# Kernel tuning notes

Hardware: AMD Instinct MI355X
Metric: run time of the kernel (lower is better)

The kernel has to match this reference:

```python
import jax, jax.numpy as jnp
import numpy as np

N, E, D = 10000, 160000, 512
H, C = 4, 128          # hidden layers: 4 heads x 128 = 512 (residual-compatible)
HF, CF = 2, 512        # final layer: 2 heads, concat=False (mean)
NEG_SLOPE = 0.2


def _gat(x, src, dst, W, a_src, a_dst, b, heads, out_c, concat):
    """PyG-style GATConv (v1 attention), no dropout (eval mode)."""
    n = x.shape[0]
    h = (x @ W).reshape(n, heads, out_c)                  # [N,H,C]
    es = (h * a_src).sum(-1)                              # [N,H]
    ed = (h * a_dst).sum(-1)                              # [N,H]
    e = jax.nn.leaky_relu(es[src] + ed[dst], NEG_SLOPE)   # [E,H]
    m = jax.ops.segment_max(e, dst, num_segments=n)       # softmax over in-edges of dst
    m = jnp.where(jnp.isfinite(m), m, 0.0)                # guard isolated nodes
    ex = jnp.exp(e - m[dst])
    den = jax.ops.segment_sum(ex, dst, num_segments=n)
    alpha = ex / (den[dst] + 1e-16)                       # [E,H]
    msg = h[src] * alpha[..., None]                       # [E,H,C]
    out = jax.ops.segment_sum(msg, dst, num_segments=n)   # [N,H,C]
    out = out.reshape(n, heads * out_c) if concat else out.mean(axis=1)
    return out + b


def setup_inputs() -> dict:
    key = jax.random.key(0)
    ks = jax.random.split(key, 16)
    s = 0.05
    return {
        "graph": jax.random.normal(ks[0], (N, D), jnp.float32),
        "edge_index": jax.random.randint(ks[1], (2, E), 0, N, dtype=jnp.int32),
        "W1": jax.random.normal(ks[2], (D, H * C), jnp.float32) * s,
        "as1": jax.random.normal(ks[3], (H, C), jnp.float32) * s,
        "ad1": jax.random.normal(ks[4], (H, C), jnp.float32) * s,
        "b1": jnp.zeros((H * C,), jnp.float32),
        "W2": jax.random.normal(ks[5], (H * C, H * C), jnp.float32) * s,
        "as2": jax.random.normal(ks[6], (H, C), jnp.float32) * s,
        "ad2": jax.random.normal(ks[7], (H, C), jnp.float32) * s,
        "b2": jnp.zeros((H * C,), jnp.float32),
        "W3": jax.random.normal(ks[8], (H * C, HF * CF), jnp.float32) * s,
        "as3": jax.random.normal(ks[9], (HF, CF), jnp.float32) * s,
        "ad3": jax.random.normal(ks[10], (HF, CF), jnp.float32) * s,
        "b3": jnp.zeros((CF,), jnp.float32),
    }


def reference(graph, edge_index, W1, as1, ad1, b1, W2, as2, ad2, b2, W3, as3, ad3, b3):
    src, dst = edge_index[0], edge_index[1]
    # layer_size=2: conv1 + convs[0] with ELU+residual, convs[1] (concat=False) residual only
    x = jax.nn.elu(_gat(graph, src, dst, W1, as1, ad1, b1, H, C, True) + graph)
    x = jax.nn.elu(_gat(x, src, dst, W2, as2, ad2, b2, H, C, True) + x)
    x = _gat(x, src, dst, W3, as3, ad3, b3, HF, CF, False) + x
    return x
```

## Files before the change

kernel.cpp:

```cpp
#include <hip/hip_runtime.h>
#include <hip/hip_bf16.h>
#include <hip/hip_fp16.h>
#include <cstddef>
#include <cstdint>


typedef _Float16 half8 __attribute__((ext_vector_type(8)));
typedef _Float16 half4v __attribute__((ext_vector_type(4)));
typedef _Float16 half2v __attribute__((ext_vector_type(2)));
typedef float floatx4 __attribute__((ext_vector_type(4)));

#define AS1(p) ((const __attribute__((address_space(1))) void*)(p))
#define AS3(p) ((__attribute__((address_space(3))) void*)(p))


__global__ void count_deg(const int* __restrict__ dst, int* __restrict__ deg, int E) {
    int e = blockIdx.x * blockDim.x + threadIdx.x;
    if (e < E) atomicAdd(&deg[dst[e]], 1);
}

__global__ void scan_kernel(const int* __restrict__ deg, int* __restrict__ row_start,
                            int* __restrict__ cursor, int n) {
    __shared__ int wsum[16];
    __shared__ int carry_s;
    int tid = threadIdx.x;
    int wave = tid >> 6, lane = tid & 63;
    if (tid == 0) { carry_s = 0; row_start[0] = 0; }
    __syncthreads();
    for (int base = 0; base < n; base += 1024) {
        int i = base + tid;
        int v = (i < n) ? deg[i] : 0;
        int x = v;
#pragma unroll
        for (int off = 1; off < 64; off <<= 1) {
            int t = __shfl_up(x, off);
            if (lane >= off) x += t;
        }
        if (lane == 63) wsum[wave] = x;
        __syncthreads();
        if (wave == 0 && lane < 16) {
            int w = wsum[lane];
#pragma unroll
            for (int off = 1; off < 16; off <<= 1) {
                int t = __shfl_up(w, off);
                if (lane >= off) w += t;
            }
            wsum[lane] = w;
        }
        __syncthreads();
        int carry = carry_s;
        int incl = x + (wave ? wsum[wave - 1] : 0) + carry;
        if (i < n) { row_start[i + 1] = incl; cursor[i] = incl - v; }
        __syncthreads();
        if (tid == 1023) carry_s = incl;
        __syncthreads();
    }
}

__global__ void scatter_edges(const int* __restrict__ src, const int* __restrict__ dst,
                              int* __restrict__ cursor, int* __restrict__ srcs, int E) {
    int e = blockIdx.x * blockDim.x + threadIdx.x;
    if (e < E) {
        int p = atomicAdd(&cursor[dst[e]], 1);
        srcs[p] = src[e];
    }
}


__global__ void cast_f16(const float* __restrict__ in, _Float16* __restrict__ out, int n4) {
    int i = blockIdx.x * blockDim.x + threadIdx.x;
    if (i < n4) {
        float4 v = ((const float4*)in)[i];
        half4v o = {(_Float16)v.x, (_Float16)v.y, (_Float16)v.z, (_Float16)v.w};
        ((half4v*)out)[i] = o;
    }
}

__global__ void transpose_cast_g(const float* __restrict__ in, _Float16* __restrict__ out,
                                 int R, int Cc, int in_ld, int out_ld) {
    __shared__ float t[32][33];
    int r0 = blockIdx.y * 32, c0 = blockIdx.x * 32;
    int tx = threadIdx.x, ty = threadIdx.y;
    for (int i = ty; i < 32; i += 8)
        t[i][tx] = in[(size_t)(r0 + i) * in_ld + c0 + tx];
    __syncthreads();
    for (int i = ty; i < 32; i += 8)
        out[(size_t)(c0 + i) * out_ld + r0 + tx] = (_Float16)t[tx][i];
}


#define BK 64

__global__ __launch_bounds__(256) void gemm_f16(const _Float16* __restrict__ A,
                                                const _Float16* __restrict__ Bt,
                                                _Float16* __restrict__ C,
                                                int M, int Nn, int K) {
    __shared__ _Float16 As[64 * BK];
    __shared__ _Float16 Bs[64 * BK];
    int tid = threadIdx.x;
    int lane = tid & 63, wave = tid >> 6;
    int wm = (wave & 1) * 32, wn = (wave >> 1) * 32;
    int m0 = blockIdx.y * 64, n0 = blockIdx.x * 64;
    int l15 = lane & 15, quad = lane >> 4;
    int trow = tid >> 3, tcol = tid & 7;

    floatx4 acc[2][2];
#pragma unroll
    for (int i = 0; i < 2; ++i)
#pragma unroll
        for (int j = 0; j < 2; ++j) acc[i][j] = (floatx4){0.f, 0.f, 0.f, 0.f};

    for (int k0 = 0; k0 < K; k0 += BK) {
        __syncthreads();
#pragma unroll
        for (int i = 0; i < 2; ++i) {
            int gr = m0 + i * 32 + trow; if (gr >= M) gr = M - 1;
            __builtin_amdgcn_global_load_lds(AS1(A + (size_t)gr * K + k0 + tcol * 8),
                                             AS3(As + (size_t)(i * 256 + tid) * 8), 16, 0, 0);
        }
#pragma unroll
        for (int i = 0; i < 2; ++i) {
            int gr = n0 + i * 32 + trow;
            __builtin_amdgcn_global_load_lds(AS1(Bt + (size_t)gr * K + k0 + tcol * 8),
                                             AS3(Bs + (size_t)(i * 256 + tid) * 8), 16, 0, 0);
        }
        __syncthreads();
#pragma unroll
        for (int ks = 0; ks < BK; ks += 32) {
            half8 af[2], bfr[2];
#pragma unroll
            for (int i = 0; i < 2; ++i)
                af[i] = *(const half8*)&As[(wm + i * 16 + l15) * BK + ks + quad * 8];
#pragma unroll
            for (int j = 0; j < 2; ++j)
                bfr[j] = *(const half8*)&Bs[(wn + j * 16 + l15) * BK + ks + quad * 8];
#pragma unroll
            for (int i = 0; i < 2; ++i)
#pragma unroll
                for (int j = 0; j < 2; ++j)
                    acc[i][j] = __builtin_amdgcn_mfma_f32_16x16x32_f16(af[i], bfr[j], acc[i][j], 0, 0, 0);
        }
    }
#pragma unroll
    for (int i = 0; i < 2; ++i)
#pragma unroll
        for (int j = 0; j < 2; ++j) {
            int col = n0 + wn + j * 16 + l15;
#pragma unroll
            for (int r = 0; r < 4; ++r) {
                int row = m0 + wm + i * 16 + quad * 4 + r;
                if (row < M) C[(size_t)row * Nn + col] = (_Float16)acc[i][j][r];
            }
        }
}

__global__ __launch_bounds__(256) void gemm_f16_ep(const _Float16* __restrict__ A,
                                                   const _Float16* __restrict__ Bt,
                                                   float* __restrict__ out,
                                                   const float* __restrict__ bias,
                                                   const float* __restrict__ xres,
                                                   int M, int Nn, int K) {
    __shared__ _Float16 As[64 * BK];
    __shared__ _Float16 Bs[64 * BK];
    int tid = threadIdx.x;
    int lane = tid & 63, wave = tid >> 6;
    int wm = (wave & 1) * 32, wn = (wave >> 1) * 32;
    int m0 = blockIdx.y * 64, n0 = blockIdx.x * 64;
    int l15 = lane & 15, quad = lane >> 4;
    int trow = tid >> 3, tcol = tid & 7;

    floatx4 acc[2][2];
#pragma unroll
    for (int i = 0; i < 2; ++i)
#pragma unroll
        for (int j = 0; j < 2; ++j) acc[i][j] = (floatx4){0.f, 0.f, 0.f, 0.f};

    for (int k0 = 0; k0 < K; k0 += BK) {
        __syncthreads();
#pragma unroll
        for (int i = 0; i < 2; ++i) {
            int gr = m0 + i * 32 + trow; if (gr >= M) gr = M - 1;
            __builtin_amdgcn_global_load_lds(AS1(A + (size_t)gr * K + k0 + tcol * 8),
                                             AS3(As + (size_t)(i * 256 + tid) * 8), 16, 0, 0);
        }
#pragma unroll
        for (int i = 0; i < 2; ++i) {
            int gr = n0 + i * 32 + trow;
            __builtin_amdgcn_global_load_lds(AS1(Bt + (size_t)gr * K + k0 + tcol * 8),
                                             AS3(Bs + (size_t)(i * 256 + tid) * 8), 16, 0, 0);
        }
        __syncthreads();
#pragma unroll
        for (int ks = 0; ks < BK; ks += 32) {
            half8 af[2], bfr[2];
#pragma unroll
            for (int i = 0; i < 2; ++i)
                af[i] = *(const half8*)&As[(wm + i * 16 + l15) * BK + ks + quad * 8];
#pragma unroll
            for (int j = 0; j < 2; ++j)
                bfr[j] = *(const half8*)&Bs[(wn + j * 16 + l15) * BK + ks + quad * 8];
#pragma unroll
            for (int i = 0; i < 2; ++i)
#pragma unroll
                for (int j = 0; j < 2; ++j)
                    acc[i][j] = __builtin_amdgcn_mfma_f32_16x16x32_f16(af[i], bfr[j], acc[i][j], 0, 0, 0);
        }
    }
#pragma unroll
    for (int i = 0; i < 2; ++i)
#pragma unroll
        for (int j = 0; j < 2; ++j) {
            int col = n0 + wn + j * 16 + l15;
#pragma unroll
            for (int r = 0; r < 4; ++r) {
                int row = m0 + wm + i * 16 + quad * 4 + r;
                if (row < M)
                    out[(size_t)row * Nn + col] =
                        0.5f * acc[i][j][r] + bias[col] + xres[(size_t)row * Nn + col];
            }
        }
}


__global__ void attn_coef(const _Float16* __restrict__ h, const float* __restrict__ a_src,
                          const float* __restrict__ a_dst, float* __restrict__ es,
                          float* __restrict__ ed, int NH, int Hh, int C) {
    int gw = (blockIdx.x * blockDim.x + threadIdx.x) >> 6;
    int lane = threadIdx.x & 63;
    if (gw >= NH) return;
    int hd = gw % Hh;
    const _Float16* hp = h + (size_t)gw * C;
    const float* ap = a_src + hd * C;
    const float* dp = a_dst + hd * C;
    float ss = 0.f, sd = 0.f;
    for (int c = lane; c < C; c += 64) {
        float hv = (float)hp[c];
        ss += hv * ap[c];
        sd += hv * dp[c];
    }
#pragma unroll
    for (int off = 32; off; off >>= 1) {
        ss += __shfl_down(ss, off);
        sd += __shfl_down(sd, off);
    }
    if (lane == 0) { es[gw] = ss; ed[gw] = sd; }
}

__global__ void attn_coef_shared(const _Float16* __restrict__ x, const float* __restrict__ a_src,
                                 const float* __restrict__ a_dst, float* __restrict__ es,
                                 float* __restrict__ ed, int NH, int Hh, int C) {
    int gw = (blockIdx.x * blockDim.x + threadIdx.x) >> 6;
    int lane = threadIdx.x & 63;
    if (gw >= NH) return;
    int n = gw / Hh, hd = gw - n * Hh;
    const _Float16* hp = x + (size_t)n * C;
    const float* ap = a_src + hd * C;
    const float* dp = a_dst + hd * C;
    float ss = 0.f, sd = 0.f;
    for (int c = lane; c < C; c += 64) {
        float hv = (float)hp[c];
        ss += hv * ap[c];
        sd += hv * dp[c];
    }
#pragma unroll
    for (int off = 32; off; off >>= 1) {
        ss += __shfl_down(ss, off);
        sd += __shfl_down(sd, off);
    }
    if (lane == 0) { es[gw] = ss; ed[gw] = sd; }
}

__global__ void proj_a3(const float* __restrict__ W3, const float* __restrict__ as3,
                        const float* __restrict__ ad3, float* __restrict__ wes,
                        float* __restrict__ wed) {
    int gw = (blockIdx.x * blockDim.x + threadIdx.x) >> 6;
    int lane = threadIdx.x & 63;
    int k = gw & 511, h = (gw >> 9) & 1, sel = gw >> 10;
    const float* a = (sel ? ad3 : as3) + h * 512;
    const float* row = W3 + (size_t)k * 1024 + h * 512;
    float s = 0.f;
    for (int c = lane; c < 512; c += 64) s += row[c] * a[c];
#pragma unroll
    for (int off = 32; off; off >>= 1) s += __shfl_down(s, off);
    if (lane == 0) (sel ? wed : wes)[h * 512 + k] = s;
}


template <int H>
__global__ __launch_bounds__(256) void attn_alpha_packed(
    const float* __restrict__ es, const float* __restrict__ ed,
    const int* __restrict__ row_start, const int* __restrict__ srcs,
    float* __restrict__ alpha, int Nn, int E) {
    const int EP = 64 / H;
    int wave = threadIdx.x >> 6, lane = threadIdx.x & 63;
    int n = blockIdx.x * 4 + wave;
    if (n >= Nn) return;
    int h = lane & (H - 1);
    int eslot = lane / H;
    float edn = ed[n * H + h];
    int beg = row_start[n], end = row_start[n + 1];
    float m = -INFINITY;
    for (int j0 = beg; j0 < end; j0 += EP) {
        int j = j0 + eslot;
        float e = -INFINITY;
        if (j < end) {
            e = es[srcs[j] * H + h] + edn;
            e = (e > 0.f) ? e : 0.2f * e;
            alpha[(size_t)h * E + j] = e;
        }
        m = fmaxf(m, e);
    }
#pragma unroll
    for (int off = H; off < 64; off <<= 1) m = fmaxf(m, __shfl_xor(m, off));
    float den = 0.f;
    for (int j0 = beg; j0 < end; j0 += EP) {
        int j = j0 + eslot;
        if (j < end) {
            float w = __expf(alpha[(size_t)h * E + j] - m);
            alpha[(size_t)h * E + j] = w;
            den += w;
        }
    }
#pragma unroll
    for (int off = H; off < 64; off <<= 1) den += __shfl_xor(den, off);
    float inv = 1.f / (den + 1e-16f);
    for (int j0 = beg; j0 < end; j0 += EP) {
        int j = j0 + eslot;
        if (j < end) alpha[(size_t)h * E + j] *= inv;
    }
}


__global__ __launch_bounds__(512) void aggregate3_concat(
    const _Float16* __restrict__ h, const float* __restrict__ alpha,
    const int* __restrict__ row_start, const int* __restrict__ srcs,
    const float* __restrict__ bias, const float* __restrict__ x_res,
    float* __restrict__ x_out, _Float16* __restrict__ x_out_h, int E) {
    __shared__ float red[8][512];
    int n = blockIdx.x;
    int tid = threadIdx.x;
    int slot = tid >> 6, lane = tid & 63;
    int head = lane >> 4;
    int c0 = lane * 8;
    const float* al = alpha + (size_t)head * E;
    int beg = row_start[n], end = row_start[n + 1];
    float acc[8] = {};
    int j = beg + slot;
    for (; j + 8 < end; j += 16) {
        int s0 = srcs[j], s1 = srcs[j + 8];
        float w0 = al[j], w1 = al[j + 8];
        half8 h0 = *(const half8*)&h[(size_t)s0 * 512 + c0];
        half8 h1 = *(const half8*)&h[(size_t)s1 * 512 + c0];
#pragma unroll
        for (int k = 0; k < 8; ++k) acc[k] += w0 * (float)h0[k];
#pragma unroll
        for (int k = 0; k < 8; ++k) acc[k] += w1 * (float)h1[k];
    }
    if (j < end) {
        int s = srcs[j];
        float w = al[j];
        half8 hv = *(const half8*)&h[(size_t)s * 512 + c0];
#pragma unroll
        for (int k = 0; k < 8; ++k) acc[k] += w * (float)hv[k];
    }
#pragma unroll
    for (int k = 0; k < 8; ++k) red[slot][c0 + k] = acc[k];
    __syncthreads();
    int c = tid;
    size_t base = (size_t)n * 512 + c;
    float v = red[0][c] + red[1][c] + red[2][c] + red[3][c] +
              red[4][c] + red[5][c] + red[6][c] + red[7][c] + bias[c] + x_res[base];
    v = (v > 0.f) ? v : expm1f(v);
    x_out[base] = v;
    x_out_h[base] = (_Float16)v;
}


__global__ __launch_bounds__(512) void aggregate_x_dual(
    const _Float16* __restrict__ x, const float* __restrict__ alpha,
    const int* __restrict__ row_start, const int* __restrict__ srcs,
    _Float16* __restrict__ y, int E) {
    __shared__ float red[8][1024];
    int n = blockIdx.x;
    int tid = threadIdx.x;
    int slot = tid >> 6, lane = tid & 63;
    int c0 = lane * 8;
    const float* al0 = alpha;
    const float* al1 = alpha + E;
    int beg = row_start[n], end = row_start[n + 1];
    float a0[8] = {}, a1[8] = {};
    int j = beg + slot;
    for (; j + 8 < end; j += 16) {
        int s0 = srcs[j], s1 = srcs[j + 8];
        float u0 = al0[j], v0 = al1[j];
        float u1 = al0[j + 8], v1 = al1[j + 8];
        half8 h0 = *(const half8*)&x[(size_t)s0 * 512 + c0];
        half8 h1 = *(const half8*)&x[(size_t)s1 * 512 + c0];
#pragma unroll
        for (int k = 0; k < 8; ++k) {
            float f = (float)h0[k];
            a0[k] += u0 * f;
            a1[k] += v0 * f;
        }
#pragma unroll
        for (int k = 0; k < 8; ++k) {
            float f = (float)h1[k];
            a0[k] += u1 * f;
            a1[k] += v1 * f;
        }
    }
    if (j < end) {
        int s = srcs[j];
        float u = al0[j], v = al1[j];
        half8 hv = *(const half8*)&x[(size_t)s * 512 + c0];
#pragma unroll
        for (int k = 0; k < 8; ++k) {
            float f = (float)hv[k];
            a0[k] += u * f;
            a1[k] += v * f;
        }
    }
#pragma unroll
    for (int k = 0; k < 8; ++k) {
        red[slot][c0 + k] = a0[k];
        red[slot][512 + c0 + k] = a1[k];
    }
    __syncthreads();
    int c = tid * 2;
    half2v o;
#pragma unroll
    for (int k = 0; k < 2; ++k) {
        float s = red[0][c + k] + red[1][c + k] + red[2][c + k] + red[3][c + k] +
                  red[4][c + k] + red[5][c + k] + red[6][c + k] + red[7][c + k];
        o[k] = (_Float16)s;
    }
    *(half2v*)&y[(size_t)n * 1024 + c] = o;
}


extern "C" void kernel_launch(void* const* d_in, const int* in_sizes, int n_in,
                              void* d_out, int out_size, void* d_ws, size_t ws_size,
                              hipStream_t stream) {
    const float* graph = (const float*)d_in[0];
    const int* edge_index = (const int*)d_in[1];
    const float* W1 = (const float*)d_in[2];
    const float* as1 = (const float*)d_in[3];
    const float* ad1 = (const float*)d_in[4];
    const float* b1 = (const float*)d_in[5];
    const float* W2 = (const float*)d_in[6];
    const float* as2 = (const float*)d_in[7];
    const float* ad2 = (const float*)d_in[8];
    const float* b2 = (const float*)d_in[9];
    const float* W3 = (const float*)d_in[10];
    const float* as3 = (const float*)d_in[11];
    const float* ad3 = (const float*)d_in[12];
    const float* b3 = (const float*)d_in[13];

    const int D = 512;
    int N = in_sizes[0] / D;
    int E = in_sizes[1] / 2;
    const int* src = edge_index;
    const int* dst = edge_index + E;

    char* p = (char*)d_ws;
    auto carve = [&](size_t bytes) {
        void* r = (void*)p;
        p += (bytes + 255) & ~(size_t)255;
        return r;
    };
    _Float16* Ah  = (_Float16*)carve((size_t)N * 512 * 2);
    _Float16* Wt  = (_Float16*)carve((size_t)512 * 512 * 2);
    _Float16* Bt3 = (_Float16*)carve((size_t)512 * 1024 * 2);
    _Float16* h_h = (_Float16*)carve((size_t)N * 1024 * 2);
    float* x1     = (float*)carve((size_t)N * 512 * 4);
    float* x2     = (float*)carve((size_t)N * 512 * 4);
    float* es     = (float*)carve((size_t)N * 4 * 4);
    float* ed     = (float*)carve((size_t)N * 4 * 4);
    float* alpha  = (float*)carve((size_t)4 * E * 4);
    float* wes3   = (float*)carve((size_t)2 * 512 * 4);
    float* wed3   = (float*)carve((size_t)2 * 512 * 4);
    int* deg      = (int*)carve((size_t)N * 4);
    int* cur      = (int*)carve((size_t)N * 4);
    int* row_st   = (int*)carve((size_t)(N + 1) * 4);
    int* srcs     = (int*)carve((size_t)E * 4);

    hipMemsetAsync(deg, 0, (size_t)N * 4, stream);
    count_deg<<<(E + 255) / 256, 256, 0, stream>>>(dst, deg, E);
    scan_kernel<<<1, 1024, 0, stream>>>(deg, row_st, cur, N);
    scatter_edges<<<(E + 255) / 256, 256, 0, stream>>>(src, dst, cur, srcs, E);

    cast_f16<<<(N * 512 / 4 + 255) / 256, 256, 0, stream>>>(graph, Ah, N * 512 / 4);

    dim3 tblk(32, 8);
    int nblk4 = (N + 3) / 4;
    int mblk = (N + 63) / 64;
    transpose_cast_g<<<dim3(16, 16), tblk, 0, stream>>>(W1, Wt, 512, 512, 512, 512);
    gemm_f16<<<dim3(512 / 64, mblk), 256, 0, stream>>>(Ah, Wt, h_h, N, 512, 512);
    attn_coef<<<(N * 4 + 3) / 4, 256, 0, stream>>>(h_h, as1, ad1, es, ed, N * 4, 4, 128);
    attn_alpha_packed<4><<<nblk4, 256, 0, stream>>>(es, ed, row_st, srcs, alpha, N, E);
    aggregate3_concat<<<N, 512, 0, stream>>>(h_h, alpha, row_st, srcs, b1, graph, x1, Ah, E);

    transpose_cast_g<<<dim3(16, 16), tblk, 0, stream>>>(W2, Wt, 512, 512, 512, 512);
    gemm_f16<<<dim3(512 / 64, mblk), 256, 0, stream>>>(Ah, Wt, h_h, N, 512, 512);
    attn_coef<<<(N * 4 + 3) / 4, 256, 0, stream>>>(h_h, as2, ad2, es, ed, N * 4, 4, 128);
    attn_alpha_packed<4><<<nblk4, 256, 0, stream>>>(es, ed, row_st, srcs, alpha, N, E);
    aggregate3_concat<<<N, 512, 0, stream>>>(h_h, alpha, row_st, srcs, b2, x1, x2, Ah, E);

    transpose_cast_g<<<dim3(16, 16), tblk, 0, stream>>>(W3, Bt3, 512, 512, 1024, 1024);
    transpose_cast_g<<<dim3(16, 16), tblk, 0, stream>>>(W3 + 512, Bt3 + 512, 512, 512, 1024, 1024);
    proj_a3<<<512, 256, 0, stream>>>(W3, as3, ad3, wes3, wed3);
    attn_coef_shared<<<(N * 2 + 3) / 4, 256, 0, stream>>>(Ah, wes3, wed3, es, ed, N * 2, 2, 512);
    attn_alpha_packed<2><<<nblk4, 256, 0, stream>>>(es, ed, row_st, srcs, alpha, N, E);
    aggregate_x_dual<<<N, 512, 0, stream>>>(Ah, alpha, row_st, srcs, h_h, E);
    gemm_f16_ep<<<dim3(512 / 64, mblk), 256, 0, stream>>>(
        h_h, Bt3, (float*)d_out, b3, x2, N, 512, 1024);
}
```

Measured before the change: 347.5 us.

## Fold attention projections into GEMM columns and defer softmax normalization to aggregation

Precomputes W·a_src and W·a_dst as extra rows of the transposed weight, so the hidden-layer GEMM emits es/ed directly and the separate attention-coefficient kernels go away. The softmax kernel now writes the per-node denominator instead of renormalizing every alpha, and the aggregation kernels divide by it. Layer-3 coefficients are computed inside the layer-2 aggregation epilogue. The fp32 intermediate activations are dropped in favor of fp16 residuals, which saves bandwidth at some cost in precision. All weight preprocessing is grouped up front into a single projection kernel.

```diff
diff --git a/kernel.cpp b/kernel.cpp
--- a/kernel.cpp
+++ b/kernel.cpp
@@ -77,7 +77,7 @@
 }
 
 __global__ void transpose_cast_g(const float* __restrict__ in, _Float16* __restrict__ out,
-                                 int R, int Cc, int in_ld, int out_ld) {
+                                 int in_ld, int out_ld) {
     __shared__ float t[32][33];
     int r0 = blockIdx.y * 32, c0 = blockIdx.x * 32;
     int tx = threadIdx.x, ty = threadIdx.y;
@@ -88,13 +88,61 @@
         out[(size_t)(c0 + i) * out_ld + r0 + tx] = (_Float16)t[tx][i];
 }
 
+__global__ void proj_all(const float* __restrict__ W1, const float* __restrict__ as1,
+                         const float* __restrict__ ad1,
+                         const float* __restrict__ W2, const float* __restrict__ as2,
+                         const float* __restrict__ ad2,
+                         const float* __restrict__ W3, const float* __restrict__ as3,
+                         const float* __restrict__ ad3,
+                         _Float16* __restrict__ Wt1, _Float16* __restrict__ Wt2,
+                         float* __restrict__ wes3, float* __restrict__ wed3) {
+    int w = (blockIdx.x * blockDim.x + threadIdx.x) >> 6;
+    int lane = threadIdx.x & 63;
+    if (w < 8192) {
+        int layer = w >> 12;
+        int idx = w & 4095;
+        int d = idx & 511, hh = (idx >> 9) & 3, sel = idx >> 11;
+        const float* W = layer ? W2 : W1;
+        const float* a = layer ? (sel ? ad2 : as2) : (sel ? ad1 : as1);
+        const float* row = W + (size_t)d * 512 + hh * 128;
+        const float* av = a + hh * 128;
+        float s = 0.f;
+        s += row[lane] * av[lane];
+        s += row[lane + 64] * av[lane + 64];
+#pragma unroll
+        for (int off = 32; off; off >>= 1) s += __shfl_down(s, off);
+        if (lane == 0) {
+            _Float16* Wt = layer ? Wt2 : Wt1;
+            Wt[(size_t)(512 + sel * 4 + hh) * 512 + d] = (_Float16)s;
+        }
+    } else if (w < 10240) {
+        int idx = w - 8192;
+        int k = idx & 511, hh = (idx >> 9) & 1, sel = idx >> 10;
+        const float* a = (sel ? ad3 : as3) + hh * 512;
+        const float* row = W3 + (size_t)k * 1024 + hh * 512;
+        float s = 0.f;
+        for (int c = lane; c < 512; c += 64) s += row[c] * a[c];
+#pragma unroll
+        for (int off = 32; off; off >>= 1) s += __shfl_down(s, off);
+        if (lane == 0) (sel ? wed3 : wes3)[hh * 512 + k] = s;
+    } else if (w < 11136) {
+        int z = (w - 10240) * 64 + lane;
+        int layer = z / 28672;
+        int rem = z - layer * 28672;
+        int row = 520 + rem / 512, col = rem & 511;
+        (layer ? Wt2 : Wt1)[(size_t)row * 512 + col] = (_Float16)0.f;
+    }
+}
+
 
 #define BK 64
 
-__global__ __launch_bounds__(256) void gemm_f16(const _Float16* __restrict__ A,
-                                                const _Float16* __restrict__ Bt,
-                                                _Float16* __restrict__ C,
-                                                int M, int Nn, int K) {
+__global__ __launch_bounds__(256) void gemm_f16_att(const _Float16* __restrict__ A,
+                                                    const _Float16* __restrict__ Bt,
+                                                    _Float16* __restrict__ Hout,
+                                                    float* __restrict__ es,
+                                                    float* __restrict__ ed,
+                                                    int M, int K) {
     __shared__ _Float16 As[64 * BK];
     __shared__ _Float16 Bs[64 * BK];
     int tid = threadIdx.x;
@@ -149,7 +197,12 @@
 #pragma unroll
             for (int r = 0; r < 4; ++r) {
                 int row = m0 + wm + i * 16 + quad * 4 + r;
-                if (row < M) C[(size_t)row * Nn + col] = (_Float16)acc[i][j][r];
+                if (row < M) {
+                    float v = acc[i][j][r];
+                    if (col < 512) Hout[(size_t)row * 512 + col] = (_Float16)v;
+                    else if (col < 516) es[row * 4 + col - 512] = v;
+                    else if (col < 520) ed[row * 4 + col - 516] = v;
+                }
             }
         }
 }
@@ -158,7 +211,7 @@
                                                    const _Float16* __restrict__ Bt,
                                                    float* __restrict__ out,
                                                    const float* __restrict__ bias,
-                                                   const float* __restrict__ xres,
+                                                   const _Float16* __restrict__ xres,
                                                    int M, int Nn, int K) {
     __shared__ _Float16 As[64 * BK];
     __shared__ _Float16 Bs[64 * BK];
@@ -216,81 +269,17 @@
                 int row = m0 + wm + i * 16 + quad * 4 + r;
                 if (row < M)
                     out[(size_t)row * Nn + col] =
-                        0.5f * acc[i][j][r] + bias[col] + xres[(size_t)row * Nn + col];
+                        0.5f * acc[i][j][r] + bias[col] + (float)xres[(size_t)row * Nn + col];
             }
         }
 }
 
 
-__global__ void attn_coef(const _Float16* __restrict__ h, const float* __restrict__ a_src,
-                          const float* __restrict__ a_dst, float* __restrict__ es,
-                          float* __restrict__ ed, int NH, int Hh, int C) {
-    int gw = (blockIdx.x * blockDim.x + threadIdx.x) >> 6;
-    int lane = threadIdx.x & 63;
-    if (gw >= NH) return;
-    int hd = gw % Hh;
-    const _Float16* hp = h + (size_t)gw * C;
-    const float* ap = a_src + hd * C;
-    const float* dp = a_dst + hd * C;
-    float ss = 0.f, sd = 0.f;
-    for (int c = lane; c < C; c += 64) {
-        float hv = (float)hp[c];
-        ss += hv * ap[c];
-        sd += hv * dp[c];
-    }
-#pragma unroll
-    for (int off = 32; off; off >>= 1) {
-        ss += __shfl_down(ss, off);
-        sd += __shfl_down(sd, off);
-    }
-    if (lane == 0) { es[gw] = ss; ed[gw] = sd; }
-}
-
-__global__ void attn_coef_shared(const _Float16* __restrict__ x, const float* __restrict__ a_src,
-                                 const float* __restrict__ a_dst, float* __restrict__ es,
-                                 float* __restrict__ ed, int NH, int Hh, int C) {
-    int gw = (blockIdx.x * blockDim.x + threadIdx.x) >> 6;
-    int lane = threadIdx.x & 63;
-    if (gw >= NH) return;
-    int n = gw / Hh, hd = gw - n * Hh;
-    const _Float16* hp = x + (size_t)n * C;
-    const float* ap = a_src + hd * C;
-    const float* dp = a_dst + hd * C;
-    float ss = 0.f, sd = 0.f;
-    for (int c = lane; c < C; c += 64) {
-        float hv = (float)hp[c];
-        ss += hv * ap[c];
-        sd += hv * dp[c];
-    }
-#pragma unroll
-    for (int off = 32; off; off >>= 1) {
-        ss += __shfl_down(ss, off);
-        sd += __shfl_down(sd, off);
-    }
-    if (lane == 0) { es[gw] = ss; ed[gw] = sd; }
-}
-
-__global__ void proj_a3(const float* __restrict__ W3, const float* __restrict__ as3,
-                        const float* __restrict__ ad3, float* __restrict__ wes,
-                        float* __restrict__ wed) {
-    int gw = (blockIdx.x * blockDim.x + threadIdx.x) >> 6;
-    int lane = threadIdx.x & 63;
-    int k = gw & 511, h = (gw >> 9) & 1, sel = gw >> 10;
-    const float* a = (sel ? ad3 : as3) + h * 512;
-    const float* row = W3 + (size_t)k * 1024 + h * 512;
-    float s = 0.f;
-    for (int c = lane; c < 512; c += 64) s += row[c] * a[c];
-#pragma unroll
-    for (int off = 32; off; off >>= 1) s += __shfl_down(s, off);
-    if (lane == 0) (sel ? wed : wes)[h * 512 + k] = s;
-}
-
-
 template <int H>
-__global__ __launch_bounds__(256) void attn_alpha_packed(
+__global__ __launch_bounds__(256) void attn_alpha2(
     const float* __restrict__ es, const float* __restrict__ ed,
     const int* __restrict__ row_start, const int* __restrict__ srcs,
-    float* __restrict__ alpha, int Nn, int E) {
+    float* __restrict__ alpha, float* __restrict__ den, int Nn, int E) {
     const int EP = 64 / H;
     int wave = threadIdx.x >> 6, lane = threadIdx.x & 63;
     int n = blockIdx.x * 4 + wave;
@@ -312,31 +301,32 @@
     }
 #pragma unroll
     for (int off = H; off < 64; off <<= 1) m = fmaxf(m, __shfl_xor(m, off));
-    float den = 0.f;
+    float dsum = 0.f;
     for (int j0 = beg; j0 < end; j0 += EP) {
         int j = j0 + eslot;
         if (j < end) {
             float w = __expf(alpha[(size_t)h * E + j] - m);
             alpha[(size_t)h * E + j] = w;
-            den += w;
-        }
-    }
-#pragma unroll
-    for (int off = H; off < 64; off <<= 1) den += __shfl_xor(den, off);
-    float inv = 1.f / (den + 1e-16f);
-    for (int j0 = beg; j0 < end; j0 += EP) {
-        int j = j0 + eslot;
-        if (j < end) alpha[(size_t)h * E + j] *= inv;
-    }
-}
-
-
-__global__ __launch_bounds__(512) void aggregate3_concat(
+            dsum += w;
+        }
+    }
+#pragma unroll
+    for (int off = H; off < 64; off <<= 1) dsum += __shfl_xor(dsum, off);
+    if (lane < H) den[n * H + lane] = dsum;
+}
+
+
+template <bool RES32, bool COEF3>
+__global__ __launch_bounds__(512) void aggregate4_concat(
     const _Float16* __restrict__ h, const float* __restrict__ alpha,
+    const float* __restrict__ den,
     const int* __restrict__ row_start, const int* __restrict__ srcs,
-    const float* __restrict__ bias, const float* __restrict__ x_res,
-    float* __restrict__ x_out, _Float16* __restrict__ x_out_h, int E) {
+    const float* __restrict__ bias, const float* __restrict__ xres32,
+    const _Float16* __restrict__ xres16, _Float16* __restrict__ x_out_h,
+    const float* __restrict__ wes3, const float* __restrict__ wed3,
+    float* __restrict__ es3, float* __restrict__ ed3, int E) {
     __shared__ float red[8][512];
+    __shared__ float csum[8][4];
     int n = blockIdx.x;
     int tid = threadIdx.x;
     int slot = tid >> 6, lane = tid & 63;
@@ -367,17 +357,46 @@
     for (int k = 0; k < 8; ++k) red[slot][c0 + k] = acc[k];
     __syncthreads();
     int c = tid;
+    float invden = 1.f / (den[n * 4 + (c >> 7)] + 1e-16f);
+    float s = red[0][c] + red[1][c] + red[2][c] + red[3][c] +
+              red[4][c] + red[5][c] + red[6][c] + red[7][c];
     size_t base = (size_t)n * 512 + c;
-    float v = red[0][c] + red[1][c] + red[2][c] + red[3][c] +
-              red[4][c] + red[5][c] + red[6][c] + red[7][c] + bias[c] + x_res[base];
+    float res = RES32 ? xres32[base] : (float)xres16[base];
+    float v = s * invden + bias[c] + res;
     v = (v > 0.f) ? v : expm1f(v);
-    x_out[base] = v;
     x_out_h[base] = (_Float16)v;
+    if (COEF3) {
+        float t0 = v * wes3[c], t1 = v * wes3[512 + c];
+        float t2 = v * wed3[c], t3 = v * wed3[512 + c];
+#pragma unroll
+        for (int off = 32; off; off >>= 1) {
+            t0 += __shfl_down(t0, off);
+            t1 += __shfl_down(t1, off);
+            t2 += __shfl_down(t2, off);
+            t3 += __shfl_down(t3, off);
+        }
+        if (lane == 0) {
+            csum[slot][0] = t0; csum[slot][1] = t1;
+            csum[slot][2] = t2; csum[slot][3] = t3;
+        }
+        __syncthreads();
+        if (tid == 0) {
+            float a0 = 0, a1 = 0, a2 = 0, a3 = 0;
+#pragma unroll
+            for (int w = 0; w < 8; ++w) {
+                a0 += csum[w][0]; a1 += csum[w][1];
+                a2 += csum[w][2]; a3 += csum[w][3];
+            }
+            es3[n * 2] = a0; es3[n * 2 + 1] = a1;
+            ed3[n * 2] = a2; ed3[n * 2 + 1] = a3;
+        }
+    }
 }
 
 
 __global__ __launch_bounds__(512) void aggregate_x_dual(
     const _Float16* __restrict__ x, const float* __restrict__ alpha,
+    const float* __restrict__ den,
     const int* __restrict__ row_start, const int* __restrict__ srcs,
     _Float16* __restrict__ y, int E) {
     __shared__ float red[8][1024];
@@ -426,13 +445,16 @@
         red[slot][512 + c0 + k] = a1[k];
     }
     __syncthreads();
+    float invd0 = 1.f / (den[n * 2] + 1e-16f);
+    float invd1 = 1.f / (den[n * 2 + 1] + 1e-16f);
     int c = tid * 2;
+    float inv = (c < 512) ? invd0 : invd1;
     half2v o;
 #pragma unroll
     for (int k = 0; k < 2; ++k) {
         float s = red[0][c + k] + red[1][c + k] + red[2][c + k] + red[3][c + k] +
                   red[4][c + k] + red[5][c + k] + red[6][c + k] + red[7][c + k];
-        o[k] = (_Float16)s;
+        o[k] = (_Float16)(s * inv);
     }
     *(half2v*)&y[(size_t)n * 1024 + c] = o;
 }
@@ -468,21 +490,21 @@
         p += (bytes + 255) & ~(size_t)255;
         return r;
     };
-    _Float16* Ah  = (_Float16*)carve((size_t)N * 512 * 2);
-    _Float16* Wt  = (_Float16*)carve((size_t)512 * 512 * 2);
-    _Float16* Bt3 = (_Float16*)carve((size_t)512 * 1024 * 2);
-    _Float16* h_h = (_Float16*)carve((size_t)N * 1024 * 2);
-    float* x1     = (float*)carve((size_t)N * 512 * 4);
-    float* x2     = (float*)carve((size_t)N * 512 * 4);
-    float* es     = (float*)carve((size_t)N * 4 * 4);
-    float* ed     = (float*)carve((size_t)N * 4 * 4);
-    float* alpha  = (float*)carve((size_t)4 * E * 4);
-    float* wes3   = (float*)carve((size_t)2 * 512 * 4);
-    float* wed3   = (float*)carve((size_t)2 * 512 * 4);
-    int* deg      = (int*)carve((size_t)N * 4);
-    int* cur      = (int*)carve((size_t)N * 4);
-    int* row_st   = (int*)carve((size_t)(N + 1) * 4);
-    int* srcs     = (int*)carve((size_t)E * 4);
+    _Float16* Ah   = (_Float16*)carve((size_t)N * 512 * 2);
+    _Float16* Wt1  = (_Float16*)carve((size_t)576 * 512 * 2);
+    _Float16* Wt2  = (_Float16*)carve((size_t)576 * 512 * 2);
+    _Float16* Bt3  = (_Float16*)carve((size_t)512 * 1024 * 2);
+    _Float16* h_h  = (_Float16*)carve((size_t)N * 1024 * 2);
+    float* es      = (float*)carve((size_t)N * 4 * 4);
+    float* ed      = (float*)carve((size_t)N * 4 * 4);
+    float* den     = (float*)carve((size_t)N * 4 * 4);
+    float* alpha   = (float*)carve((size_t)4 * E * 4);
+    float* wes3    = (float*)carve((size_t)2 * 512 * 4);
+    float* wed3    = (float*)carve((size_t)2 * 512 * 4);
+    int* deg       = (int*)carve((size_t)N * 4);
+    int* cur       = (int*)carve((size_t)N * 4);
+    int* row_st    = (int*)carve((size_t)(N + 1) * 4);
+    int* srcs      = (int*)carve((size_t)E * 4);
 
     hipMemsetAsync(deg, 0, (size_t)N * 4, stream);
     count_deg<<<(E + 255) / 256, 256, 0, stream>>>(dst, deg, E);
@@ -490,28 +512,30 @@
     scatter_edges<<<(E + 255) / 256, 256, 0, stream>>>(src, dst, cur, srcs, E);
 
     cast_f16<<<(N * 512 / 4 + 255) / 256, 256, 0, stream>>>(graph, Ah, N * 512 / 4);
-
     dim3 tblk(32, 8);
+    transpose_cast_g<<<dim3(16, 16), tblk, 0, stream>>>(W1, Wt1, 512, 512);
+    transpose_cast_g<<<dim3(16, 16), tblk, 0, stream>>>(W2, Wt2, 512, 512);
+    transpose_cast_g<<<dim3(16, 16), tblk, 0, stream>>>(W3, Bt3, 1024, 1024);
+    transpose_cast_g<<<dim3(16, 16), tblk, 0, stream>>>(W3 + 512, Bt3 + 512, 1024, 1024);
+    proj_all<<<2784, 256, 0, stream>>>(W1, as1, ad1, W2, as2, ad2, W3, as3, ad3,
+                                       Wt1, Wt2, wes3, wed3);
+
     int nblk4 = (N + 3) / 4;
     int mblk = (N + 63) / 64;
-    transpose_cast_g<<<dim3(16, 16), tblk, 0, stream>>>(W1, Wt, 512, 512, 512, 512);
-    gemm_f16<<<dim3(512 / 64, mblk), 256, 0, stream>>>(Ah, Wt, h_h, N, 512, 512);
-    attn_coef<<<(N * 4 + 3) / 4, 256, 0, stream>>>(h_h, as1, ad1, es, ed, N * 4, 4, 128);
-    attn_alpha_packed<4><<<nblk4, 256, 0, stream>>>(es, ed, row_st, srcs, alpha, N, E);
-    aggregate3_concat<<<N, 512, 0, stream>>>(h_h, alpha, row_st, srcs, b1, graph, x1, Ah, E);
-
-    transpose_cast_g<<<dim3(16, 16), tblk, 0, stream>>>(W2, Wt, 512, 512, 512, 512);
-    gemm_f16<<<dim3(512 / 64, mblk), 256, 0, stream>>>(Ah, Wt, h_h, N, 512, 512);
-    attn_coef<<<(N * 4 + 3) / 4, 256, 0, stream>>>(h_h, as2, ad2, es, ed, N * 4, 4, 128);
-    attn_alpha_packed<4><<<nblk4, 256, 0, stream>>>(es, ed, row_st, srcs, alpha, N, E);
-    aggregate3_concat<<<N, 512, 0, stream>>>(h_h, alpha, row_st, srcs, b2, x1, x2, Ah, E);
-
-    transpose_cast_g<<<dim3(16, 16), tblk, 0, stream>>>(W3, Bt3, 512, 512, 1024, 1024);
-    transpose_cast_g<<<dim3(16, 16), tblk, 0, stream>>>(W3 + 512, Bt3 + 512, 512, 512, 1024, 1024);
-    proj_a3<<<512, 256, 0, stream>>>(W3, as3, ad3, wes3, wed3);
-    attn_coef_shared<<<(N * 2 + 3) / 4, 256, 0, stream>>>(Ah, wes3, wed3, es, ed, N * 2, 2, 512);
-    attn_alpha_packed<2><<<nblk4, 256, 0, stream>>>(es, ed, row_st, srcs, alpha, N, E);
-    aggregate_x_dual<<<N, 512, 0, stream>>>(Ah, alpha, row_st, srcs, h_h, E);
-    gemm_f16_ep<<<dim3(512 / 64, mblk), 256, 0, stream>>>(
-        h_h, Bt3, (float*)d_out, b3, x2, N, 512, 1024);
-}
+    gemm_f16_att<<<dim3(9, mblk), 256, 0, stream>>>(Ah, Wt1, h_h, es, ed, N, 512);
+    attn_alpha2<4><<<nblk4, 256, 0, stream>>>(es, ed, row_st, srcs, alpha, den, N, E);
+    aggregate4_concat<true, false><<<N, 512, 0, stream>>>(
+        h_h, alpha, den, row_st, srcs, b1, graph, nullptr, Ah,
+        nullptr, nullptr, nullptr, nullptr, E);
+
+    gemm_f16_att<<<dim3(9, mblk), 256, 0, stream>>>(Ah, Wt2, h_h, es, ed, N, 512);
+    attn_alpha2<4><<<nblk4, 256, 0, stream>>>(es, ed, row_st, srcs, alpha, den, N, E);
+    aggregate4_concat<false, true><<<N, 512, 0, stream>>>(
+        h_h, alpha, den, row_st, srcs, b2, nullptr, Ah, Ah,
+        wes3, wed3, es, ed, E);
+
+    attn_alpha2<2><<<nblk4, 256, 0, stream>>>(es, ed, row_st, srcs, alpha, den, N, E);
+    aggregate_x_dual<<<N, 512, 0, stream>>>(Ah, alpha, den, row_st, srcs, h_h, E);
+    gemm_f16_ep<<<dim3(8, mblk), 256, 0, stream>>>(
+        h_h, Bt3, (float*)d_out, b3, Ah, N, 512, 1024);
+}
```

Result: faster. 337.3 us (-3.0%).
